# Performance work log

Hardware: AMD Instinct MI355X
Metric: run time of the kernel (lower is better)

## Reference

```python
import jax, jax.numpy as jnp
import numpy as np

N, F_IN, H, C, E = 50000, 256, 4, 64, 800000
HC = H * C  # n_target_nodes = 256


def setup_inputs() -> dict:
    key = jax.random.key(0)
    ks = jax.random.split(key, 16)
    s = 1.0 / np.sqrt(F_IN)
    inp = {
        "x": jax.random.normal(ks[0], (N, F_IN), jnp.float32),
        "edge_index": jax.random.randint(ks[1], (2, E), 0, N, jnp.int64),
        "edge_attr": jax.random.uniform(ks[2], (E, 1), jnp.float32),
        "Wq": jax.random.normal(ks[3], (F_IN, HC), jnp.float32) * s,
        "bq": jnp.zeros((HC,), jnp.float32),
        "Wk": jax.random.normal(ks[4], (F_IN, HC), jnp.float32) * s,
        "bk": jnp.zeros((HC,), jnp.float32),
        "Wv": jax.random.normal(ks[5], (F_IN, HC), jnp.float32) * s,
        "bv": jnp.zeros((HC,), jnp.float32),
        "We": jax.random.normal(ks[6], (1, HC), jnp.float32),
        "be": jnp.zeros((HC,), jnp.float32),
        "Wskip": jax.random.normal(ks[7], (F_IN, HC), jnp.float32) * s,
        "bskip": jnp.zeros((HC,), jnp.float32),
        "gn_weight": jnp.ones((HC,), jnp.float32),
        "gn_bias": jnp.zeros((HC,), jnp.float32),
        "gn_mean_scale": jnp.ones((HC,), jnp.float32),
    }
    return inp


def _la_forward(x, edge_index, edge_attr, Wq, bq, Wk, bk, Wv, bv, We, be,
                Wskip, bskip, gn_weight, gn_bias, gn_mean_scale):
    n = x.shape[0]
    src, dst = edge_index[0], edge_index[1]  # message src(j) -> dst(i)
    q = (x @ Wq + bq).reshape(n, H, C)
    k = (x @ Wk + bk).reshape(n, H, C)
    v = (x @ Wv + bv).reshape(n, H, C)
    e = (edge_attr @ We + be).reshape(-1, H, C)  # [E,H,C]

    k_j = k[src] + e                              # [E,H,C]
    alpha = jnp.einsum('ehc,ehc->eh', q[dst], k_j) / jnp.sqrt(jnp.float32(C))
    # edge-softmax over incoming edges of each dst node
    amax = jax.ops.segment_max(alpha, dst, num_segments=n)      # [N,H]
    ex = jnp.exp(alpha - amax[dst])
    denom = jax.ops.segment_sum(ex, dst, num_segments=n)        # [N,H]
    attn = ex / (denom[dst] + 1e-16)                            # [E,H]

    msg = (v[src] + e) * attn[:, :, None]                       # [E,H,C]
    out = jax.ops.segment_sum(msg, dst, num_segments=n).reshape(n, HC)
    out = out + x @ Wskip + bskip                               # root/skip

    # GraphNorm (single graph batch)
    mean = out.mean(axis=0)
    centered = out - gn_mean_scale * mean
    var = (centered * centered).mean(axis=0)
    out = centered / jnp.sqrt(var + 1e-5) * gn_weight + gn_bias

    out = jax.nn.relu(out)
    xt = out.T @ out                                            # [HC,HC]
    xt_min, xt_max = jnp.min(xt), jnp.max(xt)
    xt = (xt - xt_min) / (xt_max - xt_min + 1e-8)
    return xt


def reference(x, edge_index, edge_attr, Wq, bq, Wk, bk, Wv, bv, We, be,
              Wskip, bskip, gn_weight, gn_bias, gn_mean_scale):
    return _la_forward(x, edge_index, edge_attr, Wq, bq, Wk, bk, Wv, bv,
                       We, be, Wskip, bskip, gn_weight, gn_bias, gn_mean_scale)
```

## Files before the change

kernel.cpp:

```cpp
#include <hip/hip_runtime.h>
#include <math.h>


typedef float f32x4 __attribute__((ext_vector_type(4)));
typedef short s16x8 __attribute__((ext_vector_type(8)));

static __device__ __forceinline__ unsigned short f2bf(float f) {
    unsigned int u = __float_as_uint(f);
    unsigned int r = u + 0x7FFFu + ((u >> 16) & 1u);
    return (unsigned short)(r >> 16);
}
static __device__ __forceinline__ float bf2f(unsigned short u) {
    return __uint_as_float(((unsigned int)u) << 16);
}
static __device__ __forceinline__ float blo(unsigned int u) {
    return __uint_as_float(u << 16);
}
static __device__ __forceinline__ float bhi(unsigned int u) {
    return __uint_as_float(u & 0xffff0000u);
}

#define LOG2E_8 0.18033688011112042f

__global__ __launch_bounds__(256) void la_prep(
    const float* __restrict__ x, int total4,
    const float* __restrict__ Wq, const float* __restrict__ Wk,
    const float* __restrict__ Wv, const float* __restrict__ Ws,
    const float* __restrict__ bq, const float* __restrict__ bk,
    const float* __restrict__ bv, const float* __restrict__ bs,
    unsigned short* __restrict__ wt, float* __restrict__ bcat,
    const int* __restrict__ dst, int e,
    int* __restrict__ deg, int* __restrict__ pos,
    unsigned short* __restrict__ xb)
{
    __shared__ float T[64][68];
    const int bid = blockIdx.x;
    const int t = threadIdx.x;

    if (bid < 64) {
        const int m  = bid >> 4;
        const int kt = (bid >> 2) & 3, ct = bid & 3;
        const int k0 = kt * 64, c0 = ct * 64;
        const float* W = (m == 0) ? Wq : (m == 1) ? Wk : (m == 2) ? Wv : Ws;
        const float* B = (m == 0) ? bq : (m == 1) ? bk : (m == 2) ? bv : bs;
#pragma unroll
        for (int it = 0; it < 4; ++it) {
            int s = it * 256 + t;
            int r = s >> 4;
            int q = (s & 15) * 4;
            float4 v = *(const float4*)(W + (size_t)(k0 + r) * 256 + c0 + q);
            T[r][q + 0] = v.x; T[r][q + 1] = v.y;
            T[r][q + 2] = v.z; T[r][q + 3] = v.w;
        }
        __syncthreads();
#pragma unroll
        for (int it = 0; it < 4; ++it) {
            int s = it * 256 + t;
            int c = s >> 4;
            int kq = (s & 15) * 4;
            ushort4 o;
            o.x = f2bf(T[kq + 0][c]); o.y = f2bf(T[kq + 1][c]);
            o.z = f2bf(T[kq + 2][c]); o.w = f2bf(T[kq + 3][c]);
            *(ushort4*)(wt + (size_t)(m * 256 + c0 + c) * 256 + k0 + kq) = o;
        }
        if (kt == 0 && t < 64) bcat[m * 256 + c0 + t] = B[c0 + t];
    } else if (bid < 1088) {
        int i = (bid - 64) * 256 + t;
        const int stride = 1024 * 256;
        for (; i < e; i += stride)
            pos[i] = atomicAdd(&deg[dst[i]], 1);
    } else {
        int i = (bid - 1088) * 256 + t;
        const int stride = 2048 * 256;
        for (; i < total4; i += stride) {
            float4 v = ((const float4*)x)[i];
            ushort4 o;
            o.x = f2bf(v.x); o.y = f2bf(v.y); o.z = f2bf(v.z); o.w = f2bf(v.w);
            ((ushort4*)xb)[i] = o;
        }
    }
}

__global__ __launch_bounds__(256) void la_gemm_mfma(
    const unsigned short* __restrict__ xb, const unsigned short* __restrict__ wt,
    const float* __restrict__ bcat,
    unsigned short* __restrict__ qarr, unsigned short* __restrict__ kv,
    unsigned short* __restrict__ skiparr, int n)
{
    __shared__ __align__(16) unsigned short As[128 * 40];
    __shared__ __align__(16) unsigned short Bs[128 * 40];

    const int row0 = blockIdx.x * 128;
    const int col0 = blockIdx.y * 128;
    const int msel = blockIdx.y >> 1;
    const int t = threadIdx.x;
    const int l = t & 63;
    const int w = t >> 6;
    const int wr = w >> 1, wc = w & 1;
    const int l15 = l & 15, l4 = l >> 4;

    f32x4 acc[4][4];
#pragma unroll
    for (int i = 0; i < 4; ++i)
#pragma unroll
        for (int j = 0; j < 4; ++j) acc[i][j] = (f32x4){0.f, 0.f, 0.f, 0.f};

    for (int k0 = 0; k0 < 256; k0 += 32) {
#pragma unroll
        for (int c2 = 0; c2 < 2; ++c2) {
            int chunk = t + c2 * 256;
            int r  = chunk >> 2;
            int ko = (chunk & 3) * 8;
            int ga = row0 + r;
            s16x8 va = (s16x8){0,0,0,0,0,0,0,0};
            if (ga < n) va = *(const s16x8*)(xb + (size_t)ga * 256 + k0 + ko);
            *(s16x8*)(As + r * 40 + ko) = va;
            int gb = col0 + r;
            s16x8 vb = *(const s16x8*)(wt + (size_t)gb * 256 + k0 + ko);
            *(s16x8*)(Bs + r * 40 + ko) = vb;
        }
        __syncthreads();
        s16x8 af[4], bfr[4];
#pragma unroll
        for (int f = 0; f < 4; ++f) {
            af[f]  = *(const s16x8*)(As + (wr * 64 + f * 16 + l15) * 40 + l4 * 8);
            bfr[f] = *(const s16x8*)(Bs + (wc * 64 + f * 16 + l15) * 40 + l4 * 8);
        }
#pragma unroll
        for (int fm = 0; fm < 4; ++fm)
#pragma unroll
            for (int fn = 0; fn < 4; ++fn)
                acc[fm][fn] = __builtin_amdgcn_mfma_f32_16x16x32_bf16(
                    af[fm], bfr[fn], acc[fm][fn], 0, 0, 0);
        __syncthreads();
    }

#pragma unroll
    for (int fm = 0; fm < 4; ++fm) {
#pragma unroll
        for (int fn = 0; fn < 4; ++fn) {
            int gc = col0 + wc * 64 + fn * 16 + l15;
            int c  = gc & 255;
            float bb = bcat[gc];
#pragma unroll
            for (int j = 0; j < 4; ++j) {
                int gr = row0 + wr * 64 + fm * 16 + l4 * 4 + j;
                if (gr >= n) continue;
                unsigned short val = f2bf(acc[fm][fn][j] + bb);
                if (msel == 0) {
                    qarr[(size_t)gr * 256 + c] = val;
                } else if (msel == 3) {
                    skiparr[(size_t)gr * 256 + c] = val;
                } else {
                    int hh = c >> 6, ch = c & 63;
                    size_t idx = (size_t)gr * 512 + hh * 128 + (ch >> 2) * 8
                               + (ch & 3) + ((msel == 2) ? 4 : 0);
                    kv[idx] = val;
                }
            }
        }
    }
}

__global__ void la_chunksum(const int* __restrict__ deg, int n, int* __restrict__ part)
{
    int b = blockIdx.x, t = threadIdx.x;
    int i = b * 256 + t;
    int v = (i < n) ? deg[i] : 0;
#pragma unroll
    for (int mask = 32; mask >= 1; mask >>= 1) v += __shfl_xor(v, mask);
    __shared__ int ws[4];
    if ((t & 63) == 0) ws[t >> 6] = v;
    __syncthreads();
    if (t == 0) part[b] = ws[0] + ws[1] + ws[2] + ws[3];
}

__global__ void la_scanfinal(const int* __restrict__ deg, int n,
                             const int* __restrict__ part, int* __restrict__ offs,
                             int e)
{
    int b = blockIdx.x, t = threadIdx.x;
    int pv = (t < b) ? part[t] : 0;
#pragma unroll
    for (int mask = 32; mask >= 1; mask >>= 1) pv += __shfl_xor(pv, mask);
    __shared__ int pws[4];
    if ((t & 63) == 0) pws[t >> 6] = pv;
    __syncthreads();
    const int base = pws[0] + pws[1] + pws[2] + pws[3];

    int i = b * 256 + t;
    int d = (i < n) ? deg[i] : 0;
    int v = d;
#pragma unroll
    for (int o = 1; o < 64; o <<= 1) {
        int u = __shfl_up(v, o);
        if ((t & 63) >= o) v += u;
    }
    __shared__ int wt[4];
    if ((t & 63) == 63) wt[t >> 6] = v;
    __syncthreads();
    int add = 0;
    for (int wv = 0; wv < (t >> 6); ++wv) add += wt[wv];
    int excl = v + add - d + base;
    if (i < n) offs[i] = excl;
    if (b == 0 && t == 0) offs[n] = e;
}

__global__ void la_scatter2(const int* __restrict__ src, const int* __restrict__ dst,
                            const float* __restrict__ ea,
                            const int* __restrict__ pos,
                            const int* __restrict__ offs, int e,
                            uint2* __restrict__ rec)
{
    int i = blockIdx.x * blockDim.x + threadIdx.x;
    int stride = gridDim.x * blockDim.x;
    for (; i < e; i += stride) {
        int d = dst[i];
        int p = offs[d] + pos[i];
        rec[p] = make_uint2((unsigned int)src[i], __float_as_uint(ea[i]));
    }
}

__global__ __launch_bounds__(256) void la_attn4(
    const unsigned short* __restrict__ qarr,
    const unsigned short* __restrict__ kv,
    const unsigned short* __restrict__ skiparr,
    const uint2* __restrict__ rec,
    const int* __restrict__ offs,
    const float* __restrict__ We, const float* __restrict__ be,
    unsigned short* __restrict__ outb)
{
    const int node = blockIdx.x;
    const int t = threadIdx.x;
    const int h = t >> 6;
    const int l = t & 63;
    const int quarter = l >> 4;
    const int lc = l & 15;
    const int cb = h * 64 + lc * 4;

    uint2 qp = *(const uint2*)(qarr + (size_t)node * 256 + cb);
    const float q0 = blo(qp.x), q1 = bhi(qp.x);
    const float q2 = blo(qp.y), q3 = bhi(qp.y);
    float4 we4 = *(const float4*)(We + cb);
    float4 be4 = *(const float4*)(be + cb);

    float pw = fmaf(q3, we4.w, fmaf(q2, we4.z, fmaf(q1, we4.y, q0 * we4.x)));
    float pb = fmaf(q3, be4.w, fmaf(q2, be4.z, fmaf(q1, be4.y, q0 * be4.x)));
#pragma unroll
    for (int mask = 1; mask <= 8; mask <<= 1) {
        pw += __shfl_xor(pw, mask);
        pb += __shfl_xor(pb, mask);
    }
    const float qWe8 = pw * LOG2E_8;
    const float qbe8 = pb * LOG2E_8;

    const int start = offs[node], end = offs[node + 1];
    const int koff = h * 128 + lc * 8;

    float lsA = 0.f, SfA = 0.f, a0A = 0.f, a1A = 0.f, a2A = 0.f, a3A = 0.f;
    float lsB = 0.f, SfB = 0.f, a0B = 0.f, a1B = 0.f, a2B = 0.f, a3B = 0.f;

    for (int j0 = start; j0 < end; j0 += 8) {
        int ja = j0 + quarter;
        int jb = j0 + 4 + quarter;
        bool va = (ja < end), vb = (jb < end);
        int jja = va ? ja : j0;
        int jjb = vb ? jb : j0;
        uint2 ra = rec[jja];
        uint2 rb = rec[jjb];
        uint4 kva = *(const uint4*)(kv + (((size_t)(int)ra.x) << 9) + koff);
        uint4 kvb = *(const uint4*)(kv + (((size_t)(int)rb.x) << 9) + koff);
        float eaa = __uint_as_float(ra.y);
        float eab = __uint_as_float(rb.y);

        float da = fmaf(q3, bhi(kva.y), fmaf(q2, blo(kva.y),
                   fmaf(q1, bhi(kva.x), q0 * blo(kva.x))));
        float db = fmaf(q3, bhi(kvb.y), fmaf(q2, blo(kvb.y),
                   fmaf(q1, bhi(kvb.x), q0 * blo(kvb.x))));
#pragma unroll
        for (int mask = 1; mask <= 8; mask <<= 1) {
            da += __shfl_xor(da, mask);
            db += __shfl_xor(db, mask);
        }
        float aLa = fmaf(da, LOG2E_8, fmaf(eaa, qWe8, qbe8));
        float aLb = fmaf(db, LOG2E_8, fmaf(eab, qWe8, qbe8));
        aLa = va ? aLa : -INFINITY;
        aLb = vb ? aLb : -INFINITY;
        float fa = exp2f(aLa);
        float fb = exp2f(aLb);

        lsA += fa;               lsB += fb;
        SfA = fmaf(fa, eaa, SfA); SfB = fmaf(fb, eab, SfB);
        a0A = fmaf(fa, blo(kva.z), a0A); a0B = fmaf(fb, blo(kvb.z), a0B);
        a1A = fmaf(fa, bhi(kva.z), a1A); a1B = fmaf(fb, bhi(kvb.z), a1B);
        a2A = fmaf(fa, blo(kva.w), a2A); a2B = fmaf(fb, blo(kvb.w), a2B);
        a3A = fmaf(fa, bhi(kva.w), a3A); a3B = fmaf(fb, bhi(kvb.w), a3B);
    }

    float lsum = lsA + lsB, Sfa = SfA + SfB;
    float a0 = a0A + a0B, a1 = a1A + a1B, a2 = a2A + a2B, a3 = a3A + a3B;

#pragma unroll
    for (int mask = 16; mask <= 32; mask <<= 1) {
        lsum += __shfl_xor(lsum, mask);
        Sfa  += __shfl_xor(Sfa,  mask);
        a0   += __shfl_xor(a0,   mask);
        a1   += __shfl_xor(a1,   mask);
        a2   += __shfl_xor(a2,   mask);
        a3   += __shfl_xor(a3,   mask);
    }

    if (quarter == 0) {
        float inv = 1.f / (lsum + 1e-16f);
        uint2 sp = *(const uint2*)(skiparr + (size_t)node * 256 + cb);
        ushort4 o;
        o.x = f2bf(fmaf(we4.x, Sfa, fmaf(be4.x, lsum, a0)) * inv + blo(sp.x));
        o.y = f2bf(fmaf(we4.y, Sfa, fmaf(be4.y, lsum, a1)) * inv + bhi(sp.x));
        o.z = f2bf(fmaf(we4.z, Sfa, fmaf(be4.z, lsum, a2)) * inv + blo(sp.y));
        o.w = f2bf(fmaf(we4.w, Sfa, fmaf(be4.w, lsum, a3)) * inv + bhi(sp.y));
        *(ushort4*)(outb + (size_t)node * 256 + cb) = o;
    }
}

__global__ __launch_bounds__(256) void la_colsum(
    const unsigned short* __restrict__ outb, float* __restrict__ cs,
    float* __restrict__ cs2, int n)
{
    const int col = threadIdx.x;
    const int r0 = blockIdx.x * 64;
    const int rend = (r0 + 64 < n) ? r0 + 64 : n;
    float s = 0.f, s2 = 0.f;
    for (int r = r0; r < rend; ++r) {
        float vv = bf2f(outb[(size_t)r * 256 + col]);
        s += vv;
        s2 = fmaf(vv, vv, s2);
    }
    atomicAdd(&cs[col], s);
    atomicAdd(&cs2[col], s2);
}

__global__ __launch_bounds__(256) void la_gram_mfma(
    const unsigned short* __restrict__ outb,
    const float* __restrict__ cs, const float* __restrict__ cs2,
    const float* __restrict__ gnw, const float* __restrict__ gnb,
    const float* __restrict__ gms,
    float* __restrict__ xt, int n, int kchunk)
{
    __shared__ __align__(16) unsigned int Ta[128 * 20];
    __shared__ __align__(16) unsigned int Tb[128 * 20];

    const int bx = blockIdx.x;
    const int kc   = bx / 3;
    const int tile = bx - kc * 3;
    const int i0 = (tile == 2) ? 128 : 0;
    const int j0 = (tile == 0) ? 0 : 128;
    const bool diag = (tile != 1);
    const int kbeg = kc * kchunk;
    if (kbeg >= n) return;
    const int kend = (kbeg + kchunk < n) ? kbeg + kchunk : n;

    const int t = threadIdx.x;
    const int l = t & 63, w = t >> 6;
    const int wr = w >> 1, wc = w & 1;
    const int l15 = l & 15, l4 = l >> 4;

    const int kp  = t >> 4;
    const int cg8 = t & 15;

    const float invn = 1.f / (float)n;
    float Ai[8], Bi[8], Aj[8], Bj[8];
#pragma unroll
    for (int j = 0; j < 8; ++j) {
        {
            int ci = i0 + cg8 * 8 + j;
            float mean = cs[ci] * invn;
            float m2   = cs2[ci] * invn;
            float s    = gms[ci];
            float var  = m2 - 2.f * s * mean * mean + s * s * mean * mean;
            float a    = gnw[ci] / sqrtf(var + 1e-5f);
            Ai[j] = a; Bi[j] = gnb[ci] - s * mean * a;
        }
        {
            int cj = j0 + cg8 * 8 + j;
            float mean = cs[cj] * invn;
            float m2   = cs2[cj] * invn;
            float s    = gms[cj];
            float var  = m2 - 2.f * s * mean * mean + s * s * mean * mean;
            float a    = gnw[cj] / sqrtf(var + 1e-5f);
            Aj[j] = a; Bj[j] = gnb[cj] - s * mean * a;
        }
    }

    f32x4 acc[4][4];
#pragma unroll
    for (int i = 0; i < 4; ++i)
#pragma unroll
        for (int j = 0; j < 4; ++j) acc[i][j] = (f32x4){0.f, 0.f, 0.f, 0.f};

    const int nsteps = (kend - kbeg + 31) >> 5;
    for (int ks = 0; ks < nsteps; ++ks) {
        const int gr0 = kbeg + ks * 32 + kp * 2;
        const bool v0 = (gr0 < kend), v1 = (gr0 + 1 < kend);

        {
            uint4 u0 = make_uint4(0,0,0,0), u1 = make_uint4(0,0,0,0);
            if (v0) u0 = *(const uint4*)(outb + (size_t)gr0 * 256 + i0 + cg8 * 8);
            if (v1) u1 = *(const uint4*)(outb + (size_t)(gr0+1) * 256 + i0 + cg8 * 8);
            float xs[8] = {blo(u0.x),bhi(u0.x),blo(u0.y),bhi(u0.y),
                           blo(u0.z),bhi(u0.z),blo(u0.w),bhi(u0.w)};
            float ys[8] = {blo(u1.x),bhi(u1.x),blo(u1.y),bhi(u1.y),
                           blo(u1.z),bhi(u1.z),blo(u1.w),bhi(u1.w)};
#pragma unroll
            for (int j = 0; j < 8; ++j) {
                float r0 = v0 ? fmaxf(fmaf(xs[j], Ai[j], Bi[j]), 0.f) : 0.f;
                float r1 = v1 ? fmaxf(fmaf(ys[j], Ai[j], Bi[j]), 0.f) : 0.f;
                int c = cg8 * 8 + j;
                unsigned int u = (unsigned int)f2bf(r0)
                               | ((unsigned int)f2bf(r1) << 16);
                Ta[c * 20 + (kp ^ (((c >> 3) & 3) << 2))] = u;
            }
        }
        if (!diag) {
            uint4 u0 = make_uint4(0,0,0,0), u1 = make_uint4(0,0,0,0);
            if (v0) u0 = *(const uint4*)(outb + (size_t)gr0 * 256 + j0 + cg8 * 8);
            if (v1) u1 = *(const uint4*)(outb + (size_t)(gr0+1) * 256 + j0 + cg8 * 8);
            float xs[8] = {blo(u0.x),bhi(u0.x),blo(u0.y),bhi(u0.y),
                           blo(u0.z),bhi(u0.z),blo(u0.w),bhi(u0.w)};
            float ys[8] = {blo(u1.x),bhi(u1.x),blo(u1.y),bhi(u1.y),
                           blo(u1.z),bhi(u1.z),blo(u1.w),bhi(u1.w)};
#pragma unroll
            for (int j = 0; j < 8; ++j) {
                float r0 = v0 ? fmaxf(fmaf(xs[j], Aj[j], Bj[j]), 0.f) : 0.f;
                float r1 = v1 ? fmaxf(fmaf(ys[j], Aj[j], Bj[j]), 0.f) : 0.f;
                int c = cg8 * 8 + j;
                unsigned int u = (unsigned int)f2bf(r0)
                               | ((unsigned int)f2bf(r1) << 16);
                Tb[c * 20 + (kp ^ (((c >> 3) & 3) << 2))] = u;
            }
        }
        __syncthreads();

        const unsigned int* TB = diag ? Ta : Tb;
        s16x8 af[4], bfr[4];
#pragma unroll
        for (int f = 0; f < 4; ++f) {
            int ca = wr * 64 + f * 16 + l15;
            af[f] = *(const s16x8*)(Ta + ca * 20 + ((l4 * 4) ^ (((ca >> 3) & 3) << 2)));
            int cb2 = wc * 64 + f * 16 + l15;
            bfr[f] = *(const s16x8*)(TB + cb2 * 20 + ((l4 * 4) ^ (((cb2 >> 3) & 3) << 2)));
        }
#pragma unroll
        for (int fm = 0; fm < 4; ++fm)
#pragma unroll
            for (int fn = 0; fn < 4; ++fn)
                acc[fm][fn] = __builtin_amdgcn_mfma_f32_16x16x32_bf16(
                    af[fm], bfr[fn], acc[fm][fn], 0, 0, 0);
        __syncthreads();
    }

#pragma unroll
    for (int fm = 0; fm < 4; ++fm)
#pragma unroll
        for (int fn = 0; fn < 4; ++fn) {
            int col = j0 + wc * 64 + fn * 16 + l15;
#pragma unroll
            for (int j = 0; j < 4; ++j) {
                int row = i0 + wr * 64 + fm * 16 + l4 * 4 + j;
                float vv = acc[fm][fn][j];
                atomicAdd(&xt[(size_t)row * 256 + col], vv);
                if (tile == 1)
                    atomicAdd(&xt[(size_t)col * 256 + row], vv);
            }
        }
}

__global__ __launch_bounds__(256) void la_minmax_part(
    const float* __restrict__ xt, float* __restrict__ mmp)
{
    const int b = blockIdx.x, t = threadIdx.x;
    float mn = INFINITY, mx = -INFINITY;
#pragma unroll
    for (int k = 0; k < 2; ++k) {
        float4 v = ((const float4*)xt)[b * 512 + k * 256 + t];
        mn = fminf(mn, fminf(fminf(v.x, v.y), fminf(v.z, v.w)));
        mx = fmaxf(mx, fmaxf(fmaxf(v.x, v.y), fmaxf(v.z, v.w)));
    }
#pragma unroll
    for (int mask = 32; mask >= 1; mask >>= 1) {
        mn = fminf(mn, __shfl_xor(mn, mask));
        mx = fmaxf(mx, __shfl_xor(mx, mask));
    }
    __shared__ float smn[4], smx[4];
    if ((t & 63) == 0) { smn[t >> 6] = mn; smx[t >> 6] = mx; }
    __syncthreads();
    if (t == 0) {
        mn = fminf(fminf(smn[0], smn[1]), fminf(smn[2], smn[3]));
        mx = fmaxf(fmaxf(smx[0], smx[1]), fmaxf(smx[2], smx[3]));
        mmp[b * 2]     = mn;
        mmp[b * 2 + 1] = mx;
    }
}

__global__ void la_norm(float* __restrict__ xt, const float* __restrict__ mmp)
{
    float mn = INFINITY, mx = -INFINITY;
#pragma unroll
    for (int i = 0; i < 32; ++i) {
        mn = fminf(mn, mmp[i * 2]);
        mx = fmaxf(mx, mmp[i * 2 + 1]);
    }
    float inv = 1.f / (mx - mn + 1e-8f);
    int i = blockIdx.x * blockDim.x + threadIdx.x;
    xt[i] = (xt[i] - mn) * inv;
}

extern "C" void kernel_launch(void* const* d_in, const int* in_sizes, int n_in,
                              void* d_out, int out_size, void* d_ws, size_t ws_size,
                              hipStream_t stream)
{
    const float* x   = (const float*)d_in[0];
    const int*   ei  = (const int*)  d_in[1];
    const float* ea  = (const float*)d_in[2];
    const float* Wq  = (const float*)d_in[3];
    const float* bq  = (const float*)d_in[4];
    const float* Wk  = (const float*)d_in[5];
    const float* bk  = (const float*)d_in[6];
    const float* Wv  = (const float*)d_in[7];
    const float* bv  = (const float*)d_in[8];
    const float* We  = (const float*)d_in[9];
    const float* be  = (const float*)d_in[10];
    const float* Ws  = (const float*)d_in[11];
    const float* bs  = (const float*)d_in[12];
    const float* gnw = (const float*)d_in[13];
    const float* gnb = (const float*)d_in[14];
    const float* gms = (const float*)d_in[15];

    const int n = in_sizes[0] / 256;
    const int e = in_sizes[1] / 2;
    const int* srcI = ei;
    const int* dstI = ei + e;

    char* ws = (char*)d_ws;
    size_t off = 0;
    auto take = [&](size_t bytes) -> void* {
        void* p = (void*)(ws + off);
        off += (bytes + 255) & ~(size_t)255;
        return p;
    };
    int*   deg    = (int*)  take((size_t)n * 4);
    float* cs     = (float*)take(256 * 4);
    float* cs2    = (float*)take(256 * 4);
    size_t zero_bytes = off;

    unsigned short* xb    = (unsigned short*)take((size_t)n * 256 * 2);
    unsigned short* wtbuf = (unsigned short*)take((size_t)1024 * 256 * 2);
    float*          bcat  = (float*)take(1024 * 4);
    unsigned short* qarr  = (unsigned short*)take((size_t)n * 256 * 2);
    unsigned short* kv    = (unsigned short*)take((size_t)n * 512 * 2);
    unsigned short* skipb = (unsigned short*)take((size_t)n * 256 * 2);
    unsigned short* outb  = (unsigned short*)take((size_t)n * 256 * 2);
    int*   pos    = (int*)  take((size_t)e * 4);
    int*   offs   = (int*)  take((size_t)(n + 1) * 4);
    int*   part   = (int*)  take(256 * 4);
    uint2* csrR   = (uint2*)take((size_t)e * 8);
    float* mmp    = (float*)take(64 * 4);
    (void)ws_size; (void)n_in; (void)out_size;

    float* xt = (float*)d_out;

    hipMemsetAsync(deg, 0, zero_bytes, stream);
    hipMemsetAsync(xt,  0, (size_t)65536 * 4, stream);

    la_prep<<<3136, 256, 0, stream>>>(x, n * 64,
                                      Wq, Wk, Wv, Ws, bq, bk, bv, bs,
                                      wtbuf, bcat, dstI, e, deg, pos, xb);

    dim3 gg((n + 127) / 128, 8);
    la_gemm_mfma<<<gg, 256, 0, stream>>>(xb, wtbuf, bcat, qarr, kv, skipb, n);

    const int nchunk = (n + 255) / 256;
    la_chunksum <<<nchunk, 256, 0, stream>>>(deg, n, part);
    la_scanfinal<<<nchunk, 256, 0, stream>>>(deg, n, part, offs, e);
    la_scatter2 <<<1024, 256, 0, stream>>>(srcI, dstI, ea, pos, offs, e, csrR);

    la_attn4<<<n, 256, 0, stream>>>(qarr, kv, skipb, csrR, offs, We, be, outb);

    la_colsum<<<(n + 63) / 64, 256, 0, stream>>>(outb, cs, cs2, n);

    const int KSPLIT = 128;
    int kchunk = ((n + KSPLIT - 1) / KSPLIT + 31) & ~31;
    la_gram_mfma<<<3 * KSPLIT, 256, 0, stream>>>(outb, cs, cs2, gnw, gnb, gms,
                                                 xt, n, kchunk);

    la_minmax_part<<<32, 256, 0, stream>>>(xt, mmp);
    la_norm<<<256, 256, 0, stream>>>(xt, mmp);
}
```

Measured before the change: 386.1 us.

## Fuse x bf16 conversion into GEMM loads and drop separate chunksum kernel

The GEMM now reads fp32 x directly and converts it to bf16 while staging its shared-memory tile. This removes the separate conversion pass and the xb intermediate buffer. The two-kernel degree scan becomes one kernel in which each block sums all earlier degrees itself. Costs: the fp32 reads of x are repeated across the eight column blocks, and later scan blocks redo quadratic amounts of summation.

```diff
diff --git a/kernel.cpp b/kernel.cpp
--- a/kernel.cpp
+++ b/kernel.cpp
@@ -23,15 +23,13 @@
 #define LOG2E_8 0.18033688011112042f
 
 __global__ __launch_bounds__(256) void la_prep(
-    const float* __restrict__ x, int total4,
     const float* __restrict__ Wq, const float* __restrict__ Wk,
     const float* __restrict__ Wv, const float* __restrict__ Ws,
     const float* __restrict__ bq, const float* __restrict__ bk,
     const float* __restrict__ bv, const float* __restrict__ bs,
     unsigned short* __restrict__ wt, float* __restrict__ bcat,
     const int* __restrict__ dst, int e,
-    int* __restrict__ deg, int* __restrict__ pos,
-    unsigned short* __restrict__ xb)
+    int* __restrict__ deg, int* __restrict__ pos)
 {
     __shared__ float T[64][68];
     const int bid = blockIdx.x;
@@ -64,25 +62,16 @@
             *(ushort4*)(wt + (size_t)(m * 256 + c0 + c) * 256 + k0 + kq) = o;
         }
         if (kt == 0 && t < 64) bcat[m * 256 + c0 + t] = B[c0 + t];
-    } else if (bid < 1088) {
+    } else {
         int i = (bid - 64) * 256 + t;
         const int stride = 1024 * 256;
         for (; i < e; i += stride)
             pos[i] = atomicAdd(&deg[dst[i]], 1);
-    } else {
-        int i = (bid - 1088) * 256 + t;
-        const int stride = 2048 * 256;
-        for (; i < total4; i += stride) {
-            float4 v = ((const float4*)x)[i];
-            ushort4 o;
-            o.x = f2bf(v.x); o.y = f2bf(v.y); o.z = f2bf(v.z); o.w = f2bf(v.w);
-            ((ushort4*)xb)[i] = o;
-        }
     }
 }
 
 __global__ __launch_bounds__(256) void la_gemm_mfma(
-    const unsigned short* __restrict__ xb, const unsigned short* __restrict__ wt,
+    const float* __restrict__ x, const unsigned short* __restrict__ wt,
     const float* __restrict__ bcat,
     unsigned short* __restrict__ qarr, unsigned short* __restrict__ kv,
     unsigned short* __restrict__ skiparr, int n)
@@ -112,9 +101,18 @@
             int r  = chunk >> 2;
             int ko = (chunk & 3) * 8;
             int ga = row0 + r;
-            s16x8 va = (s16x8){0,0,0,0,0,0,0,0};
-            if (ga < n) va = *(const s16x8*)(xb + (size_t)ga * 256 + k0 + ko);
-            *(s16x8*)(As + r * 40 + ko) = va;
+            ushort4 alo = make_ushort4(0,0,0,0), ahi = make_ushort4(0,0,0,0);
+            if (ga < n) {
+                const float* xp = x + (size_t)ga * 256 + k0 + ko;
+                float4 v0 = *(const float4*)(xp);
+                float4 v1 = *(const float4*)(xp + 4);
+                alo.x = f2bf(v0.x); alo.y = f2bf(v0.y);
+                alo.z = f2bf(v0.z); alo.w = f2bf(v0.w);
+                ahi.x = f2bf(v1.x); ahi.y = f2bf(v1.y);
+                ahi.z = f2bf(v1.z); ahi.w = f2bf(v1.w);
+            }
+            *(ushort4*)(As + r * 40 + ko)     = alo;
+            *(ushort4*)(As + r * 40 + ko + 4) = ahi;
             int gb = col0 + r;
             s16x8 vb = *(const s16x8*)(wt + (size_t)gb * 256 + k0 + ko);
             *(s16x8*)(Bs + r * 40 + ko) = vb;
@@ -162,29 +160,17 @@
     }
 }
 
-__global__ void la_chunksum(const int* __restrict__ deg, int n, int* __restrict__ part)
+__global__ void la_scanfinal(const int* __restrict__ deg, int n,
+                             int* __restrict__ offs, int e)
 {
     int b = blockIdx.x, t = threadIdx.x;
-    int i = b * 256 + t;
-    int v = (i < n) ? deg[i] : 0;
-#pragma unroll
-    for (int mask = 32; mask >= 1; mask >>= 1) v += __shfl_xor(v, mask);
-    __shared__ int ws[4];
-    if ((t & 63) == 0) ws[t >> 6] = v;
-    __syncthreads();
-    if (t == 0) part[b] = ws[0] + ws[1] + ws[2] + ws[3];
-}
-
-__global__ void la_scanfinal(const int* __restrict__ deg, int n,
-                             const int* __restrict__ part, int* __restrict__ offs,
-                             int e)
-{
-    int b = blockIdx.x, t = threadIdx.x;
-    int pv = (t < b) ? part[t] : 0;
-#pragma unroll
-    for (int mask = 32; mask >= 1; mask >>= 1) pv += __shfl_xor(pv, mask);
+    int base_acc = 0;
+    for (int i = t; i < b * 256; i += 256) base_acc += deg[i];
+#pragma unroll
+    for (int mask = 32; mask >= 1; mask >>= 1)
+        base_acc += __shfl_xor(base_acc, mask);
     __shared__ int pws[4];
-    if ((t & 63) == 0) pws[t >> 6] = pv;
+    if ((t & 63) == 0) pws[t >> 6] = base_acc;
     __syncthreads();
     const int base = pws[0] + pws[1] + pws[2] + pws[3];
 
@@ -289,7 +275,7 @@
         float fa = exp2f(aLa);
         float fb = exp2f(aLb);
 
-        lsA += fa;               lsB += fb;
+        lsA += fa;                lsB += fb;
         SfA = fmaf(fa, eaa, SfA); SfB = fmaf(fb, eab, SfB);
         a0A = fmaf(fa, blo(kva.z), a0A); a0B = fmaf(fb, blo(kvb.z), a0B);
         a1A = fmaf(fa, bhi(kva.z), a1A); a1B = fmaf(fb, bhi(kvb.z), a1B);
@@ -552,7 +538,6 @@
     float* cs2    = (float*)take(256 * 4);
     size_t zero_bytes = off;
 
-    unsigned short* xb    = (unsigned short*)take((size_t)n * 256 * 2);
     unsigned short* wtbuf = (unsigned short*)take((size_t)1024 * 256 * 2);
     float*          bcat  = (float*)take(1024 * 4);
     unsigned short* qarr  = (unsigned short*)take((size_t)n * 256 * 2);
@@ -561,7 +546,6 @@
     unsigned short* outb  = (unsigned short*)take((size_t)n * 256 * 2);
     int*   pos    = (int*)  take((size_t)e * 4);
     int*   offs   = (int*)  take((size_t)(n + 1) * 4);
-    int*   part   = (int*)  take(256 * 4);
     uint2* csrR   = (uint2*)take((size_t)e * 8);
     float* mmp    = (float*)take(64 * 4);
     (void)ws_size; (void)n_in; (void)out_size;
@@ -571,16 +555,14 @@
     hipMemsetAsync(deg, 0, zero_bytes, stream);
     hipMemsetAsync(xt,  0, (size_t)65536 * 4, stream);
 
-    la_prep<<<3136, 256, 0, stream>>>(x, n * 64,
-                                      Wq, Wk, Wv, Ws, bq, bk, bv, bs,
-                                      wtbuf, bcat, dstI, e, deg, pos, xb);
+    la_prep<<<1088, 256, 0, stream>>>(Wq, Wk, Wv, Ws, bq, bk, bv, bs,
+                                      wtbuf, bcat, dstI, e, deg, pos);
 
     dim3 gg((n + 127) / 128, 8);
-    la_gemm_mfma<<<gg, 256, 0, stream>>>(xb, wtbuf, bcat, qarr, kv, skipb, n);
+    la_gemm_mfma<<<gg, 256, 0, stream>>>(x, wtbuf, bcat, qarr, kv, skipb, n);
 
     const int nchunk = (n + 255) / 256;
-    la_chunksum <<<nchunk, 256, 0, stream>>>(deg, n, part);
-    la_scanfinal<<<nchunk, 256, 0, stream>>>(deg, n, part, offs, e);
+    la_scanfinal<<<nchunk, 256, 0, stream>>>(deg, n, offs, e);
     la_scatter2 <<<1024, 256, 0, stream>>>(srcI, dstI, ea, pos, offs, e, csrR);
 
     la_attn4<<<n, 256, 0, stream>>>(qarr, kv, skipb, csrR, offs, We, be, outb);
```

Result: slower. 440.9 us (+14.2%).
